# Optimization experiments

Measured on AMD Instinct MI355X. Metric: run time of the kernel, lower is better.

The kernel has to match this reference:

```python
import jax, jax.numpy as jnp
import numpy as np

B, NV, F, D = 4, 100000, 200000, 64


def setup_inputs() -> dict:
    key = jax.random.key(0)
    k1, k2 = jax.random.split(key)
    verts = jax.random.normal(k1, (B, NV, D), dtype=jnp.float32)
    faces = jax.random.randint(k2, (B, F, 3), 0, NV, dtype=jnp.int64 if jax.config.jax_enable_x64 else jnp.int32)
    return {"verts": verts, "faces": faces}


def reference(verts, faces):
    # verts: [B, N, D], faces: [B, F, 3]
    Bv, N, Dv = verts.shape
    nv = N
    # offset face indices into the flattened [B*N] vertex space (block-diagonal L)
    offset = (jnp.arange(Bv) * nv).astype(faces.dtype)[:, None, None]
    f = (faces + offset).reshape(-1, 3)            # [B*F, 3]
    row = f.reshape(-1)                            # f[:, [0,1,2]]
    col = f[:, [1, 2, 0]].reshape(-1)              # next vertex in face (cyclic)
    # L (off-diag) = -(A + A^T), with multiplicity for repeated edges.
    dst = jnp.concatenate([row, col])              # accumulate into these rows
    src = jnp.concatenate([col, row])              # gather neighbor values from
    vflat = verts.reshape(-1, Dv)                  # [B*N, D]
    nbr = jax.ops.segment_sum(vflat[src], dst, num_segments=Bv * nv)          # sum_j A_sym[i,j] v[j]
    deg = jax.ops.segment_sum(jnp.ones(dst.shape[0], dtype=verts.dtype), dst,
                              num_segments=Bv * nv)                           # Lii (vertex degree)
    # x = L @ v / Lii where L = diag(deg) - A_sym
    x = (deg[:, None] * vflat - nbr) / (deg[:, None] + 1e-12)
    return x.reshape(Bv, nv, Dv)
```

## Files before the change

### kernel.cpp

```cpp
#include <hip/hip_runtime.h>

#define BB    4
#define NVV   100000
#define FFC   200000
#define DD    64
#define TOTV  (BB * NVV)
#define TOTF  (BB * FFC)
#define TOTE  (TOTF * 6)
#define NB_SCAN ((TOTV + 1023) / 1024)


__global__ __launch_bounds__(256) void ul_count(
    const int* __restrict__ faces, int* __restrict__ cnt)
{
    int t = blockIdx.x * blockDim.x + threadIdx.x;
    if (t >= TOTF) return;
    int off = (t / FFC) * NVV;
    const int* fp = faces + (size_t)t * 3;
    atomicAdd(&cnt[fp[0] + off], 2);
    atomicAdd(&cnt[fp[1] + off], 2);
    atomicAdd(&cnt[fp[2] + off], 2);
}

__global__ __launch_bounds__(256) void ul_scan1(
    const int* __restrict__ cnt, int* __restrict__ rowptr, int* __restrict__ bsum)
{
    __shared__ int s[256];
    int blk = blockIdx.x, t = threadIdx.x;
    int base = blk * 1024 + t * 4;
    int4 x = make_int4(0, 0, 0, 0);
    if (base + 3 < TOTV) x = *(const int4*)(cnt + base);
    else if (base < TOTV) {
        x.x = cnt[base];
        if (base + 1 < TOTV) x.y = cnt[base + 1];
        if (base + 2 < TOTV) x.z = cnt[base + 2];
    }
    int ts = x.x + x.y + x.z + x.w;
    s[t] = ts;
    __syncthreads();
    for (int o = 1; o < 256; o <<= 1) {
        int v = (t >= o) ? s[t - o] : 0;
        __syncthreads();
        s[t] += v;
        __syncthreads();
    }
    int ex = s[t] - ts;
    int4 r;
    r.x = ex;
    r.y = ex + x.x;
    r.z = ex + x.x + x.y;
    r.w = ex + x.x + x.y + x.z;
    if (base + 3 < TOTV) *(int4*)(rowptr + base) = r;
    else if (base < TOTV) {
        rowptr[base] = r.x;
        if (base + 1 < TOTV) rowptr[base + 1] = r.y;
        if (base + 2 < TOTV) rowptr[base + 2] = r.z;
    }
    if (t == 255) bsum[blk] = s[255];
}

__global__ __launch_bounds__(512) void ul_scan2(
    const int* __restrict__ bsum, int* __restrict__ boff)
{
    __shared__ int s[512];
    int t = threadIdx.x;
    int v = (t < NB_SCAN) ? bsum[t] : 0;
    s[t] = v;
    __syncthreads();
    for (int o = 1; o < 512; o <<= 1) {
        int w = (t >= o) ? s[t - o] : 0;
        __syncthreads();
        s[t] += w;
        __syncthreads();
    }
    if (t < NB_SCAN) boff[t] = s[t] - v;
}

__global__ __launch_bounds__(256) void ul_scan3(
    int* __restrict__ rowptr, const int* __restrict__ boff)
{
    int blk = blockIdx.x, t = threadIdx.x;
    int base = blk * 1024 + t * 4;
    int o = boff[blk];
    if (base + 3 < TOTV) {
        int4 r = *(const int4*)(rowptr + base);
        r.x += o; r.y += o; r.z += o; r.w += o;
        *(int4*)(rowptr + base) = r;
    } else if (base < TOTV) {
        rowptr[base] += o;
        if (base + 1 < TOTV) rowptr[base + 1] += o;
        if (base + 2 < TOTV) rowptr[base + 2] += o;
    }
}

__global__ __launch_bounds__(256) void ul_fill(
    const int* __restrict__ faces, int* __restrict__ rowptr, int* __restrict__ adj)
{
    int t = blockIdx.x * blockDim.x + threadIdx.x;
    if (t >= TOTF) return;
    int off = (t / FFC) * NVV;
    const int* fp = faces + (size_t)t * 3;
    int ia = fp[0] + off, ib = fp[1] + off, ic = fp[2] + off;
    int pa = atomicAdd(&rowptr[ia], 2); *(int2*)(adj + pa) = make_int2(ib, ic);
    int pb = atomicAdd(&rowptr[ib], 2); *(int2*)(adj + pb) = make_int2(ia, ic);
    int pc = atomicAdd(&rowptr[ic], 2); *(int2*)(adj + pc) = make_int2(ia, ib);
}

__global__ __launch_bounds__(256) void ul_gather(
    const float* __restrict__ v, const int* __restrict__ rowptr,
    const int* __restrict__ adj, float* __restrict__ out)
{
    int gid  = blockIdx.x * blockDim.x + threadIdx.x;
    int wid  = gid >> 6;
    int lane = gid & 63;
    if (wid >= TOTV) return;

    int start = (wid == 0) ? 0 : rowptr[wid - 1];
    int end   = rowptr[wid];
    float vi  = v[(size_t)wid * DD + lane];

    float acc = 0.0f;
    for (int base = start; base < end; base += 64) {
        int n  = min(64, end - base);
        int jv = (base + lane < end) ? adj[base + lane] : 0;
        int m = 0;
        for (; m + 8 <= n; m += 8) {
            int j0 = __shfl(jv, m);
            int j1 = __shfl(jv, m + 1);
            int j2 = __shfl(jv, m + 2);
            int j3 = __shfl(jv, m + 3);
            int j4 = __shfl(jv, m + 4);
            int j5 = __shfl(jv, m + 5);
            int j6 = __shfl(jv, m + 6);
            int j7 = __shfl(jv, m + 7);
            float a0 = v[(size_t)j0 * DD + lane];
            float a1 = v[(size_t)j1 * DD + lane];
            float a2 = v[(size_t)j2 * DD + lane];
            float a3 = v[(size_t)j3 * DD + lane];
            float a4 = v[(size_t)j4 * DD + lane];
            float a5 = v[(size_t)j5 * DD + lane];
            float a6 = v[(size_t)j6 * DD + lane];
            float a7 = v[(size_t)j7 * DD + lane];
            acc += ((a0 + a1) + (a2 + a3)) + ((a4 + a5) + (a6 + a7));
        }
        if (m + 4 <= n) {
            int j0 = __shfl(jv, m);
            int j1 = __shfl(jv, m + 1);
            int j2 = __shfl(jv, m + 2);
            int j3 = __shfl(jv, m + 3);
            float a0 = v[(size_t)j0 * DD + lane];
            float a1 = v[(size_t)j1 * DD + lane];
            float a2 = v[(size_t)j2 * DD + lane];
            float a3 = v[(size_t)j3 * DD + lane];
            acc += (a0 + a1) + (a2 + a3);
            m += 4;
        }
        for (; m < n; ++m) {
            int j = __shfl(jv, m);
            acc += v[(size_t)j * DD + lane];
        }
    }
    float dg = (float)(end - start);
    out[(size_t)wid * DD + lane] = (dg * vi - acc) / (dg + 1e-12f);
}

__global__ __launch_bounds__(256) void ul_scatter(
    const float* __restrict__ v, const int* __restrict__ faces,
    float* __restrict__ nbr, float* __restrict__ deg)
{
    int gid  = blockIdx.x * blockDim.x + threadIdx.x;
    int wid  = gid >> 6;
    int lane = gid & 63;
    if (wid >= TOTF) return;
    int off = (wid / FFC) * NVV;
    const int* fp = faces + (size_t)wid * 3;
    int ia = fp[0] + off, ib = fp[1] + off, ic = fp[2] + off;
    float va = v[(size_t)ia * DD + lane];
    float vb = v[(size_t)ib * DD + lane];
    float vc = v[(size_t)ic * DD + lane];
    atomicAdd(&nbr[(size_t)ia * DD + lane], vb + vc);
    atomicAdd(&nbr[(size_t)ib * DD + lane], va + vc);
    atomicAdd(&nbr[(size_t)ic * DD + lane], va + vb);
    if (lane < 3) {
        int t = (lane == 0) ? ia : ((lane == 1) ? ib : ic);
        atomicAdd(&deg[t], 2.0f);
    }
}

__global__ __launch_bounds__(256) void ul_finalize(
    const float4* __restrict__ v4, const float* __restrict__ deg,
    float4* __restrict__ out4, int n4)
{
    int i = blockIdx.x * blockDim.x + threadIdx.x;
    if (i >= n4) return;
    float d = deg[i >> 4];
    float4 vv = v4[i];
    float4 nb = out4[i];
    float inv = 1.0f / (d + 1e-12f);
    float4 r;
    r.x = (d * vv.x - nb.x) * inv;
    r.y = (d * vv.y - nb.y) * inv;
    r.z = (d * vv.z - nb.z) * inv;
    r.w = (d * vv.w - nb.w) * inv;
    out4[i] = r;
}


extern "C" void kernel_launch(void* const* d_in, const int* in_sizes, int n_in,
                              void* d_out, int out_size, void* d_ws, size_t ws_size,
                              hipStream_t stream)
{
    const float* verts = (const float*)d_in[0];
    const int*   faces = (const int*)d_in[1];
    float*       out   = (float*)d_out;

    size_t o_cnt    = 0;
    size_t o_rowptr = o_cnt    + ((size_t)TOTV * 4 + 255) / 256 * 256;
    size_t o_bsum   = o_rowptr + ((size_t)TOTV * 4 + 255) / 256 * 256;
    size_t o_boff   = o_bsum   + 512 * 4;
    size_t o_adj    = o_boff   + 512 * 4;
    size_t needed   = o_adj + (size_t)TOTE * 4;

    if (ws_size >= needed) {
        int* cnt    = (int*)((char*)d_ws + o_cnt);
        int* rowptr = (int*)((char*)d_ws + o_rowptr);
        int* bsum   = (int*)((char*)d_ws + o_bsum);
        int* boff   = (int*)((char*)d_ws + o_boff);
        int* adj    = (int*)((char*)d_ws + o_adj);

        hipMemsetAsync(cnt, 0, (size_t)TOTV * 4, stream);

        ul_count<<<(TOTF + 255) / 256, 256, 0, stream>>>(faces, cnt);
        ul_scan1<<<NB_SCAN, 256, 0, stream>>>(cnt, rowptr, bsum);
        ul_scan2<<<1, 512, 0, stream>>>(bsum, boff);
        ul_scan3<<<NB_SCAN, 256, 0, stream>>>(rowptr, boff);
        ul_fill <<<(TOTF + 255) / 256, 256, 0, stream>>>(faces, rowptr, adj);

        long long thr = (long long)TOTV * 64;
        ul_gather<<<(int)((thr + 255) / 256), 256, 0, stream>>>(verts, rowptr, adj, out);
    } else {
        float* deg = (float*)d_ws;
        hipMemsetAsync(d_out, 0, (size_t)out_size * sizeof(float), stream);
        hipMemsetAsync(deg,   0, (size_t)TOTV * sizeof(float), stream);
        long long thr = (long long)TOTF * 64;
        ul_scatter<<<(int)((thr + 255) / 256), 256, 0, stream>>>(verts, faces, out, deg);
        int n4 = out_size / 4;
        ul_finalize<<<(n4 + 255) / 256, 256, 0, stream>>>(
            (const float4*)verts, deg, (float4*)out, n4);
    }
}
```

Baseline: 609.2 us.

## Replicate CSR count and fill counters across blocks to reduce atomic contention

```diff
diff --git a/kernel.cpp b/kernel.cpp
--- a/kernel.cpp
+++ b/kernel.cpp
@@ -7,14 +7,16 @@
 #define TOTV  (BB * NVV)
 #define TOTF  (BB * FFC)
 #define TOTE  (TOTF * 6)
+#define NREP  8
 #define NB_SCAN ((TOTV + 1023) / 1024)
 
 
-__global__ __launch_bounds__(256) void ul_count(
-    const int* __restrict__ faces, int* __restrict__ cnt)
+__global__ __launch_bounds__(256) void ul_count8(
+    const int* __restrict__ faces, int* __restrict__ cnt8)
 {
     int t = blockIdx.x * blockDim.x + threadIdx.x;
     if (t >= TOTF) return;
+    int* cnt = cnt8 + (size_t)(blockIdx.x & (NREP - 1)) * TOTV;
     int off = (t / FFC) * NVV;
     const int* fp = faces + (size_t)t * 3;
     atomicAdd(&cnt[fp[0] + off], 2);
@@ -23,17 +25,31 @@
 }
 
 __global__ __launch_bounds__(256) void ul_scan1(
-    const int* __restrict__ cnt, int* __restrict__ rowptr, int* __restrict__ bsum)
+    const int* __restrict__ cnt8, int* __restrict__ rowptr,
+    int* __restrict__ degs, int* __restrict__ bsum)
 {
     __shared__ int s[256];
     int blk = blockIdx.x, t = threadIdx.x;
     int base = blk * 1024 + t * 4;
     int4 x = make_int4(0, 0, 0, 0);
-    if (base + 3 < TOTV) x = *(const int4*)(cnt + base);
+    if (base + 3 < TOTV) {
+        for (int r = 0; r < NREP; ++r) {
+            int4 c = *(const int4*)(cnt8 + (size_t)r * TOTV + base);
+            x.x += c.x; x.y += c.y; x.z += c.z; x.w += c.w;
+        }
+    } else if (base < TOTV) {
+        for (int r = 0; r < NREP; ++r) {
+            const int* c = cnt8 + (size_t)r * TOTV;
+            x.x += c[base];
+            if (base + 1 < TOTV) x.y += c[base + 1];
+            if (base + 2 < TOTV) x.z += c[base + 2];
+        }
+    }
+    if (base + 3 < TOTV) *(int4*)(degs + base) = x;
     else if (base < TOTV) {
-        x.x = cnt[base];
-        if (base + 1 < TOTV) x.y = cnt[base + 1];
-        if (base + 2 < TOTV) x.z = cnt[base + 2];
+        degs[base] = x.x;
+        if (base + 1 < TOTV) degs[base + 1] = x.y;
+        if (base + 2 < TOTV) degs[base + 2] = x.z;
     }
     int ts = x.x + x.y + x.z + x.w;
     s[t] = ts;
@@ -76,47 +92,66 @@
     if (t < NB_SCAN) boff[t] = s[t] - v;
 }
 
-__global__ __launch_bounds__(256) void ul_scan3(
-    int* __restrict__ rowptr, const int* __restrict__ boff)
+__global__ __launch_bounds__(256) void ul_scan3x(
+    int* __restrict__ rowptr, const int* __restrict__ boff, int* __restrict__ cnt8)
 {
     int blk = blockIdx.x, t = threadIdx.x;
     int base = blk * 1024 + t * 4;
+    if (base >= TOTV) return;
     int o = boff[blk];
     if (base + 3 < TOTV) {
         int4 r = *(const int4*)(rowptr + base);
         r.x += o; r.y += o; r.z += o; r.w += o;
         *(int4*)(rowptr + base) = r;
-    } else if (base < TOTV) {
-        rowptr[base] += o;
-        if (base + 1 < TOTV) rowptr[base + 1] += o;
-        if (base + 2 < TOTV) rowptr[base + 2] += o;
-    }
-}
-
-__global__ __launch_bounds__(256) void ul_fill(
-    const int* __restrict__ faces, int* __restrict__ rowptr, int* __restrict__ adj)
+        int run0 = r.x, run1 = r.y, run2 = r.z, run3 = r.w;
+        for (int rep = 0; rep < NREP; ++rep) {
+            int4* p = (int4*)(cnt8 + (size_t)rep * TOTV + base);
+            int4 c = *p;
+            *p = make_int4(run0, run1, run2, run3);
+            run0 += c.x; run1 += c.y; run2 += c.z; run3 += c.w;
+        }
+    } else {
+        for (int k = 0; k < 4 && base + k < TOTV; ++k) {
+            int v = rowptr[base + k] + o;
+            rowptr[base + k] = v;
+            int run = v;
+            for (int rep = 0; rep < NREP; ++rep) {
+                size_t idx = (size_t)rep * TOTV + base + k;
+                int c = cnt8[idx];
+                cnt8[idx] = run;
+                run += c;
+            }
+        }
+    }
+}
+
+__global__ __launch_bounds__(256) void ul_fill8(
+    const int* __restrict__ faces, int* __restrict__ cur, int* __restrict__ adj)
 {
     int t = blockIdx.x * blockDim.x + threadIdx.x;
     if (t >= TOTF) return;
+    int* c = cur + (size_t)(blockIdx.x & (NREP - 1)) * TOTV;
     int off = (t / FFC) * NVV;
     const int* fp = faces + (size_t)t * 3;
     int ia = fp[0] + off, ib = fp[1] + off, ic = fp[2] + off;
-    int pa = atomicAdd(&rowptr[ia], 2); *(int2*)(adj + pa) = make_int2(ib, ic);
-    int pb = atomicAdd(&rowptr[ib], 2); *(int2*)(adj + pb) = make_int2(ia, ic);
-    int pc = atomicAdd(&rowptr[ic], 2); *(int2*)(adj + pc) = make_int2(ia, ib);
+    int pa = atomicAdd(&c[ia], 2); *(int2*)(adj + pa) = make_int2(ib, ic);
+    int pb = atomicAdd(&c[ib], 2); *(int2*)(adj + pb) = make_int2(ia, ic);
+    int pc = atomicAdd(&c[ic], 2); *(int2*)(adj + pc) = make_int2(ia, ib);
 }
 
 __global__ __launch_bounds__(256) void ul_gather(
     const float* __restrict__ v, const int* __restrict__ rowptr,
-    const int* __restrict__ adj, float* __restrict__ out)
+    const int* __restrict__ degs, const int* __restrict__ adj,
+    float* __restrict__ out)
 {
     int gid  = blockIdx.x * blockDim.x + threadIdx.x;
     int wid  = gid >> 6;
     int lane = gid & 63;
     if (wid >= TOTV) return;
 
-    int start = (wid == 0) ? 0 : rowptr[wid - 1];
-    int end   = rowptr[wid];
+    int start = rowptr[wid];
+    int dgi   = degs[wid];
+    int end   = start + dgi;
     float vi  = v[(size_t)wid * DD + lane];
 
     float acc = 0.0f;
@@ -160,7 +195,7 @@
             acc += v[(size_t)j * DD + lane];
         }
     }
-    float dg = (float)(end - start);
+    float dg = (float)dgi;
     out[(size_t)wid * DD + lane] = (dg * vi - acc) / (dg + 1e-12f);
 }
 
@@ -214,30 +249,34 @@
     const int*   faces = (const int*)d_in[1];
     float*       out   = (float*)d_out;
 
-    size_t o_cnt    = 0;
-    size_t o_rowptr = o_cnt    + ((size_t)TOTV * 4 + 255) / 256 * 256;
-    size_t o_bsum   = o_rowptr + ((size_t)TOTV * 4 + 255) / 256 * 256;
+    size_t o_cnt8   = 0;
+    size_t o_rowptr = o_cnt8   + ((size_t)NREP * TOTV * 4 + 255) / 256 * 256;
+    size_t o_degs   = o_rowptr + ((size_t)TOTV * 4 + 255) / 256 * 256;
+    size_t o_bsum   = o_degs   + ((size_t)TOTV * 4 + 255) / 256 * 256;
     size_t o_boff   = o_bsum   + 512 * 4;
     size_t o_adj    = o_boff   + 512 * 4;
     size_t needed   = o_adj + (size_t)TOTE * 4;
 
     if (ws_size >= needed) {
-        int* cnt    = (int*)((char*)d_ws + o_cnt);
+        int* cnt8   = (int*)((char*)d_ws + o_cnt8);
         int* rowptr = (int*)((char*)d_ws + o_rowptr);
+        int* degs   = (int*)((char*)d_ws + o_degs);
         int* bsum   = (int*)((char*)d_ws + o_bsum);
         int* boff   = (int*)((char*)d_ws + o_boff);
         int* adj    = (int*)((char*)d_ws + o_adj);
 
-        hipMemsetAsync(cnt, 0, (size_t)TOTV * 4, stream);
-
-        ul_count<<<(TOTF + 255) / 256, 256, 0, stream>>>(faces, cnt);
-        ul_scan1<<<NB_SCAN, 256, 0, stream>>>(cnt, rowptr, bsum);
-        ul_scan2<<<1, 512, 0, stream>>>(bsum, boff);
-        ul_scan3<<<NB_SCAN, 256, 0, stream>>>(rowptr, boff);
-        ul_fill <<<(TOTF + 255) / 256, 256, 0, stream>>>(faces, rowptr, adj);
+        hipMemsetAsync(cnt8, 0, (size_t)NREP * TOTV * 4, stream);
+
+        int fillBlocks = (TOTF + 255) / 256;
+        ul_count8<<<fillBlocks, 256, 0, stream>>>(faces, cnt8);
+        ul_scan1 <<<NB_SCAN, 256, 0, stream>>>(cnt8, rowptr, degs, bsum);
+        ul_scan2 <<<1, 512, 0, stream>>>(bsum, boff);
+        ul_scan3x<<<NB_SCAN, 256, 0, stream>>>(rowptr, boff, cnt8);
+        ul_fill8 <<<fillBlocks, 256, 0, stream>>>(faces, cnt8, adj);
 
         long long thr = (long long)TOTV * 64;
-        ul_gather<<<(int)((thr + 255) / 256), 256, 0, stream>>>(verts, rowptr, adj, out);
+        ul_gather<<<(int)((thr + 255) / 256), 256, 0, stream>>>(
+            verts, rowptr, degs, adj, out);
     } else {
         float* deg = (float*)d_ws;
         hipMemsetAsync(d_out, 0, (size_t)out_size * sizeof(float), stream);
```

New measurement: 630.8 us. +3.5%, slower.

## Build CSR adjacency via partitioned bucket sort instead of global atomic fill

Applied to the files above, without the earlier changes.

```diff
diff --git a/kernel.cpp b/kernel.cpp
--- a/kernel.cpp
+++ b/kernel.cpp
@@ -4,119 +4,191 @@
 #define NVV   100000
 #define FFC   200000
 #define DD    64
-#define TOTV  (BB * NVV)
-#define TOTF  (BB * FFC)
-#define TOTE  (TOTF * 6)
-#define NB_SCAN ((TOTV + 1023) / 1024)
-
-
-__global__ __launch_bounds__(256) void ul_count(
-    const int* __restrict__ faces, int* __restrict__ cnt)
-{
-    int t = blockIdx.x * blockDim.x + threadIdx.x;
-    if (t >= TOTF) return;
-    int off = (t / FFC) * NVV;
-    const int* fp = faces + (size_t)t * 3;
-    atomicAdd(&cnt[fp[0] + off], 2);
-    atomicAdd(&cnt[fp[1] + off], 2);
-    atomicAdd(&cnt[fp[2] + off], 2);
-}
-
-__global__ __launch_bounds__(256) void ul_scan1(
-    const int* __restrict__ cnt, int* __restrict__ rowptr, int* __restrict__ bsum)
-{
-    __shared__ int s[256];
-    int blk = blockIdx.x, t = threadIdx.x;
-    int base = blk * 1024 + t * 4;
-    int4 x = make_int4(0, 0, 0, 0);
-    if (base + 3 < TOTV) x = *(const int4*)(cnt + base);
-    else if (base < TOTV) {
-        x.x = cnt[base];
-        if (base + 1 < TOTV) x.y = cnt[base + 1];
-        if (base + 2 < TOTV) x.z = cnt[base + 2];
-    }
-    int ts = x.x + x.y + x.z + x.w;
-    s[t] = ts;
-    __syncthreads();
-    for (int o = 1; o < 256; o <<= 1) {
-        int v = (t >= o) ? s[t - o] : 0;
-        __syncthreads();
-        s[t] += v;
-        __syncthreads();
-    }
-    int ex = s[t] - ts;
-    int4 r;
-    r.x = ex;
-    r.y = ex + x.x;
-    r.z = ex + x.x + x.y;
-    r.w = ex + x.x + x.y + x.z;
-    if (base + 3 < TOTV) *(int4*)(rowptr + base) = r;
-    else if (base < TOTV) {
-        rowptr[base] = r.x;
-        if (base + 1 < TOTV) rowptr[base + 1] = r.y;
-        if (base + 2 < TOTV) rowptr[base + 2] = r.z;
-    }
-    if (t == 255) bsum[blk] = s[255];
-}
-
-__global__ __launch_bounds__(512) void ul_scan2(
-    const int* __restrict__ bsum, int* __restrict__ boff)
-{
-    __shared__ int s[512];
+#define TOTV  400000
+#define TOTF  800000
+#define TOTE  4800000
+#define NPART 64
+#define VPP   6250
+#define FPW   1536
+#define NWGA  ((TOTF + FPW - 1) / FPW)
+#define ROUNDS (FPW / 256)
+#define BTHREADS 1024
+#define CHUNK 7
+
+__device__ __forceinline__ int part_of(int v) { return v / VPP; }
+
+
+__global__ __launch_bounds__(256) void ul_pcount(
+    const int* __restrict__ faces, int* __restrict__ partCnt)
+{
+    __shared__ int h[NPART];
+    int tid = threadIdx.x;
+    if (tid < NPART) h[tid] = 0;
+    __syncthreads();
+    for (int t = blockIdx.x * blockDim.x + tid; t < TOTF; t += gridDim.x * blockDim.x) {
+        int off = (t / FFC) * NVV;
+        const int* fp = faces + (size_t)t * 3;
+        int a = fp[0] + off, b = fp[1] + off, c = fp[2] + off;
+        atomicAdd(&h[part_of(a)], 2);
+        atomicAdd(&h[part_of(b)], 2);
+        atomicAdd(&h[part_of(c)], 2);
+    }
+    __syncthreads();
+    if (tid < NPART && h[tid]) atomicAdd(&partCnt[tid], h[tid]);
+}
+
+__global__ void ul_pscan(const int* __restrict__ partCnt,
+                         int* __restrict__ pbase, int* __restrict__ pcur)
+{
+    __shared__ int s[NPART];
     int t = threadIdx.x;
-    int v = (t < NB_SCAN) ? bsum[t] : 0;
+    int v = partCnt[t];
     s[t] = v;
     __syncthreads();
-    for (int o = 1; o < 512; o <<= 1) {
+    for (int o = 1; o < NPART; o <<= 1) {
         int w = (t >= o) ? s[t - o] : 0;
         __syncthreads();
         s[t] += w;
         __syncthreads();
     }
-    if (t < NB_SCAN) boff[t] = s[t] - v;
-}
-
-__global__ __launch_bounds__(256) void ul_scan3(
-    int* __restrict__ rowptr, const int* __restrict__ boff)
-{
-    int blk = blockIdx.x, t = threadIdx.x;
-    int base = blk * 1024 + t * 4;
-    int o = boff[blk];
-    if (base + 3 < TOTV) {
-        int4 r = *(const int4*)(rowptr + base);
-        r.x += o; r.y += o; r.z += o; r.w += o;
-        *(int4*)(rowptr + base) = r;
-    } else if (base < TOTV) {
-        rowptr[base] += o;
-        if (base + 1 < TOTV) rowptr[base + 1] += o;
-        if (base + 2 < TOTV) rowptr[base + 2] += o;
-    }
-}
-
-__global__ __launch_bounds__(256) void ul_fill(
-    const int* __restrict__ faces, int* __restrict__ rowptr, int* __restrict__ adj)
-{
-    int t = blockIdx.x * blockDim.x + threadIdx.x;
-    if (t >= TOTF) return;
-    int off = (t / FFC) * NVV;
-    const int* fp = faces + (size_t)t * 3;
-    int ia = fp[0] + off, ib = fp[1] + off, ic = fp[2] + off;
-    int pa = atomicAdd(&rowptr[ia], 2); *(int2*)(adj + pa) = make_int2(ib, ic);
-    int pb = atomicAdd(&rowptr[ib], 2); *(int2*)(adj + pb) = make_int2(ia, ic);
-    int pc = atomicAdd(&rowptr[ic], 2); *(int2*)(adj + pc) = make_int2(ia, ib);
+    int ex = s[t] - v;
+    pbase[t] = ex;
+    pcur[t]  = ex;
+}
+
+__global__ __launch_bounds__(256) void ul_bucket(
+    const int* __restrict__ faces, int* __restrict__ pcur, int2* __restrict__ bucket)
+{
+    __shared__ int   hist[NPART];
+    __shared__ int   offs[NPART];
+    __shared__ int   gbase[NPART];
+    __shared__ int2  ebuf[1536];
+    __shared__ short pidb[1536];
+    int tid = threadIdx.x;
+    int wg  = blockIdx.x;
+
+    for (int r = 0; r < ROUNDS; ++r) {
+        int f = wg * FPW + r * 256 + tid;
+        bool valid = f < TOTF;
+        int dsts[6], srcs[6], slot[6];
+        if (valid) {
+            int off = (f / FFC) * NVV;
+            const int* fp = faces + (size_t)f * 3;
+            int a = fp[0] + off, b = fp[1] + off, c = fp[2] + off;
+            dsts[0] = a; srcs[0] = b;  dsts[1] = a; srcs[1] = c;
+            dsts[2] = b; srcs[2] = a;  dsts[3] = b; srcs[3] = c;
+            dsts[4] = c; srcs[4] = a;  dsts[5] = c; srcs[5] = b;
+        }
+        if (tid < NPART) hist[tid] = 0;
+        __syncthreads();
+        if (valid) {
+            #pragma unroll
+            for (int k = 0; k < 6; ++k)
+                slot[k] = atomicAdd(&hist[part_of(dsts[k])], 1);
+        }
+        __syncthreads();
+        if (tid < NPART) offs[tid] = hist[tid];
+        __syncthreads();
+        for (int o = 1; o < NPART; o <<= 1) {
+            int w = 0;
+            if (tid < NPART && tid >= o) w = offs[tid - o];
+            __syncthreads();
+            if (tid < NPART) offs[tid] += w;
+            __syncthreads();
+        }
+        if (tid < NPART) {
+            offs[tid] -= hist[tid];
+            gbase[tid] = atomicAdd(&pcur[tid], hist[tid]);
+        }
+        __syncthreads();
+        int roundEdges = offs[NPART - 1] + hist[NPART - 1];
+        if (valid) {
+            #pragma unroll
+            for (int k = 0; k < 6; ++k) {
+                int p   = part_of(dsts[k]);
+                int pos = offs[p] + slot[k];
+                ebuf[pos] = make_int2(dsts[k], srcs[k]);
+                pidb[pos] = (short)p;
+            }
+        }
+        __syncthreads();
+        for (int e = tid; e < roundEdges; e += 256) {
+            int q = pidb[e];
+            bucket[gbase[q] + (e - offs[q])] = ebuf[e];
+        }
+        __syncthreads();
+    }
+}
+
+__global__ __launch_bounds__(BTHREADS) void ul_build(
+    const int2* __restrict__ bucket, const int* __restrict__ pbase,
+    const int* __restrict__ partCnt,
+    int* __restrict__ adj, int* __restrict__ rowptr, int* __restrict__ degs)
+{
+    __shared__ int lcnt[VPP];
+    __shared__ int lofs[VPP];
+    __shared__ int psum[BTHREADS];
+    int p     = blockIdx.x;
+    int tid   = threadIdx.x;
+    int vbase = p * VPP;
+    int ebase = pbase[p];
+    int ecnt  = partCnt[p];
+
+    for (int i = tid; i < VPP; i += BTHREADS) lcnt[i] = 0;
+    __syncthreads();
+    for (int e = tid; e < ecnt; e += BTHREADS)
+        atomicAdd(&lcnt[bucket[ebase + e].x - vbase], 1);
+    __syncthreads();
+
+    int base_i = tid * CHUNK;
+    int run = 0;
+    #pragma unroll
+    for (int k = 0; k < CHUNK; ++k) {
+        int i = base_i + k;
+        if (i < VPP) { int c = lcnt[i]; lofs[i] = run; run += c; }
+    }
+    psum[tid] = run;
+    __syncthreads();
+    for (int o = 1; o < BTHREADS; o <<= 1) {
+        int w = (tid >= o) ? psum[tid - o] : 0;
+        __syncthreads();
+        psum[tid] += w;
+        __syncthreads();
+    }
+    int excl = psum[tid] - run;
+    #pragma unroll
+    for (int k = 0; k < CHUNK; ++k) {
+        int i = base_i + k;
+        if (i < VPP) lofs[i] += excl;
+    }
+    __syncthreads();
+
+    for (int i = tid; i < VPP; i += BTHREADS) {
+        rowptr[vbase + i] = ebase + lofs[i];
+        degs  [vbase + i] = lcnt[i];
+    }
+    __syncthreads();
+
+    for (int e = tid; e < ecnt; e += BTHREADS) {
+        int2 ed = bucket[ebase + e];
+        int pos = atomicAdd(&lofs[ed.x - vbase], 1);
+        adj[ebase + pos] = ed.y;
+    }
 }
 
 __global__ __launch_bounds__(256) void ul_gather(
     const float* __restrict__ v, const int* __restrict__ rowptr,
-    const int* __restrict__ adj, float* __restrict__ out)
+    const int* __restrict__ degs, const int* __restrict__ adj,
+    float* __restrict__ out)
 {
     int gid  = blockIdx.x * blockDim.x + threadIdx.x;
     int wid  = gid >> 6;
     int lane = gid & 63;
     if (wid >= TOTV) return;
 
-    int start = (wid == 0) ? 0 : rowptr[wid - 1];
-    int end   = rowptr[wid];
+    int start = rowptr[wid];
+    int dgi   = degs[wid];
+    int end   = start + dgi;
     float vi  = v[(size_t)wid * DD + lane];
 
     float acc = 0.0f;
@@ -160,7 +232,7 @@
             acc += v[(size_t)j * DD + lane];
         }
     }
-    float dg = (float)(end - start);
+    float dg = (float)dgi;
     out[(size_t)wid * DD + lane] = (dg * vi - acc) / (dg + 1e-12f);
 }
 
@@ -214,30 +286,34 @@
     const int*   faces = (const int*)d_in[1];
     float*       out   = (float*)d_out;
 
-    size_t o_cnt    = 0;
-    size_t o_rowptr = o_cnt    + ((size_t)TOTV * 4 + 255) / 256 * 256;
-    size_t o_bsum   = o_rowptr + ((size_t)TOTV * 4 + 255) / 256 * 256;
-    size_t o_boff   = o_bsum   + 512 * 4;
-    size_t o_adj    = o_boff   + 512 * 4;
+    size_t o_rowptr = 0;
+    size_t o_degs   = o_rowptr + ((size_t)TOTV * 4 + 255) / 256 * 256;
+    size_t o_pcnt   = o_degs   + ((size_t)TOTV * 4 + 255) / 256 * 256;
+    size_t o_pbase  = o_pcnt   + 256;
+    size_t o_pcur   = o_pbase  + 256;
+    size_t o_adj    = o_pcur   + 256;
     size_t needed   = o_adj + (size_t)TOTE * 4;
 
     if (ws_size >= needed) {
-        int* cnt    = (int*)((char*)d_ws + o_cnt);
-        int* rowptr = (int*)((char*)d_ws + o_rowptr);
-        int* bsum   = (int*)((char*)d_ws + o_bsum);
-        int* boff   = (int*)((char*)d_ws + o_boff);
-        int* adj    = (int*)((char*)d_ws + o_adj);
-
-        hipMemsetAsync(cnt, 0, (size_t)TOTV * 4, stream);
-
-        ul_count<<<(TOTF + 255) / 256, 256, 0, stream>>>(faces, cnt);
-        ul_scan1<<<NB_SCAN, 256, 0, stream>>>(cnt, rowptr, bsum);
-        ul_scan2<<<1, 512, 0, stream>>>(bsum, boff);
-        ul_scan3<<<NB_SCAN, 256, 0, stream>>>(rowptr, boff);
-        ul_fill <<<(TOTF + 255) / 256, 256, 0, stream>>>(faces, rowptr, adj);
+        int* rowptr  = (int*)((char*)d_ws + o_rowptr);
+        int* degs    = (int*)((char*)d_ws + o_degs);
+        int* partCnt = (int*)((char*)d_ws + o_pcnt);
+        int* pbase   = (int*)((char*)d_ws + o_pbase);
+        int* pcur    = (int*)((char*)d_ws + o_pcur);
+        int* adj     = (int*)((char*)d_ws + o_adj);
+        int2* bucket = (int2*)d_out;
+
+        hipMemsetAsync(partCnt, 0, NPART * 4, stream);
+
+        ul_pcount<<<512, 256, 0, stream>>>(faces, partCnt);
+        ul_pscan <<<1, NPART, 0, stream>>>(partCnt, pbase, pcur);
+        ul_bucket<<<NWGA, 256, 0, stream>>>(faces, pcur, bucket);
+        ul_build <<<NPART, BTHREADS, 0, stream>>>(bucket, pbase, partCnt,
+                                                  adj, rowptr, degs);
 
         long long thr = (long long)TOTV * 64;
-        ul_gather<<<(int)((thr + 255) / 256), 256, 0, stream>>>(verts, rowptr, adj, out);
+        ul_gather<<<(int)((thr + 255) / 256), 256, 0, stream>>>(
+            verts, rowptr, degs, adj, out);
     } else {
         float* deg = (float*)d_ws;
         hipMemsetAsync(d_out, 0, (size_t)out_size * sizeof(float), stream);
```

After: 501.6 us. 1.21x faster.
